# Optimization experiments

Hardware: AMD Instinct MI355X
Metric: run time of the kernel (lower is better)

The kernel has to match this reference:

```python
import jax, jax.numpy as jnp
import numpy as np

ATTEN_SIZE = 5  # half-window; module-global atten_size in source (0 there is non-functional)
B, S, D_IN, HID, OUT = 8, 2048, 512, 512, 2


def _xavier(key, shape):
    fan_in, fan_out = shape
    std = (2.0 / (fan_in + fan_out)) ** 0.5
    return jax.random.normal(key, shape, dtype=jnp.float32) * std


def setup_inputs() -> dict:
    key = jax.random.key(0)
    ks = jax.random.split(key, 8)
    return {
        "x": jax.random.normal(ks[0], (B, S, D_IN), dtype=jnp.float32),
        "W1": _xavier(ks[1], (D_IN, HID)),
        "b1": jnp.zeros((1, 1, HID), dtype=jnp.float32),
        "Wq": _xavier(ks[2], (HID, HID)),
        "Wk": _xavier(ks[3], (HID, HID)),
        "Wv": _xavier(ks[4], (HID, HID)),
        "W2": _xavier(ks[5], (HID, HID)),
        "b2": jnp.zeros((1, 1, HID), dtype=jnp.float32),
        "Wfc": _xavier(ks[6], (HID, OUT)),
        "bfc": jnp.zeros((OUT,), dtype=jnp.float32),
    }


def reference(x, W1, b1, Wq, Wk, Wv, W2, b2, Wfc, bfc):
    A = ATTEN_SIZE
    Wn = 2 * A + 1
    h = jax.nn.relu(x @ W1 + b1)                      # [B,S,H]
    b, s, hd = h.shape
    padded = jnp.pad(h, ((0, 0), (A, A), (0, 0)))     # [B,S+2A,H]
    # torch pad+roll(k)+stack+slice equals reversed window: x_nei[p, j] = padded[p + 2A - j]
    idx = jnp.arange(s)[:, None] + (2 * A - jnp.arange(Wn))[None, :]  # [S,Wn]
    x_nei = padded[:, idx, :]                         # [B,S,Wn,H]
    q = h @ Wq                                        # [B,S,H]
    k = x_nei @ Wk                                    # [B,S,Wn,H]
    v = x_nei @ Wv                                    # [B,S,Wn,H]
    scale = jnp.asarray(np.sqrt(float(hd)), dtype=h.dtype)
    scores = jnp.einsum('bsh,bswh->bsw', q, k)[:, :, None, :] / scale  # [B,S,1,Wn]
    # Faithful to torch.nn.Softmax(dim=2) on a singleton dim -> all ones
    w = jax.nn.softmax(scores, axis=2)                # [B,S,1,Wn]
    aw = jnp.einsum('bsjw,bswh->bsjh', w, v).reshape(b, s, hd)  # [B,S,H]
    out = jax.nn.relu(aw @ W2 + b2) @ Wfc + bfc       # [B,S,OUT]
    return out, aw
```

## Files before the change

kernel.cpp:

```cpp
#include <hip/hip_runtime.h>
#include <stdint.h>

#define B_   8
#define S_   2048
#define HID_ 512
#define M_   (B_ * S_)
#define AW_  5

typedef __attribute__((ext_vector_type(8))) short bf16x8;
typedef __attribute__((ext_vector_type(4))) float f32x4;
typedef unsigned short u16;

__device__ __forceinline__ u16 f2bf(float f) {
    uint32_t u = __builtin_bit_cast(uint32_t, f);
    u += 0x7FFFu + ((u >> 16) & 1u);
    return (u16)(u >> 16);
}
__device__ __forceinline__ float bf2f(u16 h) {
    uint32_t u = ((uint32_t)h) << 16;
    return __builtin_bit_cast(float, u);
}

__device__ __forceinline__ void gload16(const void* g, void* l) {
    __builtin_amdgcn_global_load_lds(
        (const __attribute__((address_space(1))) void*)(uintptr_t)g,
        (__attribute__((address_space(3))) void*)(uint32_t)(uintptr_t)l,
        16, 0, 0);
}

__global__ __launch_bounds__(256) void trans2w(const float* __restrict__ S0,
                                               const float* __restrict__ S1,
                                               u16* __restrict__ D0,
                                               u16* __restrict__ D1) {
    const float* src = blockIdx.z ? S1 : S0;
    u16* dst = blockIdx.z ? D1 : D0;
    __shared__ float tile[32][33];
    const int k0 = blockIdx.y * 32, n0 = blockIdx.x * 32;
    const int tr = threadIdx.x >> 5, tc = threadIdx.x & 31;
#pragma unroll
    for (int p = 0; p < 4; ++p)
        tile[tr + p * 8][tc] = src[(long)(k0 + tr + p * 8) * HID_ + n0 + tc];
    __syncthreads();
#pragma unroll
    for (int p = 0; p < 4; ++p)
        dst[(long)(n0 + tr + p * 8) * HID_ + k0 + tc] = f2bf(tile[tc][tr + p * 8]);
}

__global__ __launch_bounds__(256, 2) void gemm1_f32a(const float* __restrict__ A,
                                                     const u16* __restrict__ Bt,
                                                     const float* __restrict__ bias,
                                                     u16* __restrict__ C) {
    __shared__ __attribute__((aligned(16))) u16 As[2][128 * 64];
    __shared__ __attribute__((aligned(16))) u16 Bs[2][128 * 64];

    const int tid = threadIdx.x;
    const int bid = blockIdx.x;
    const int swz = (bid & 7) * 64 + (bid >> 3);
    const int  bn   = (swz & 3) * 128;
    const long brow = (long)(swz >> 2) * 128;

    const int w  = tid >> 6;
    const int l  = tid & 63;
    const int wm = (w >> 1) * 64;
    const int wn = (w & 1) * 64;
    const int lr  = l & 15;
    const int lkb = (l >> 4) * 16;
    const int sw  = (lr & 7) << 4;

    const int r0 = tid >> 2;
    const int c0 = (tid & 3) * 16;
    const int r1 = 64 + r0;
    const float* ga0 = A + (brow + r0) * 512 + c0;
    const float* ga1 = A + (brow + r1) * 512 + c0;
    char* lw = (char*)&As[0][0];
    const int wb00 = r0 * 128 + ((c0 * 2 +  0) ^ ((r0 & 7) << 4));
    const int wb01 = r0 * 128 + ((c0 * 2 + 16) ^ ((r0 & 7) << 4));
    const int wb10 = r1 * 128 + ((c0 * 2 +  0) ^ ((r1 & 7) << 4));
    const int wb11 = r1 * 128 + ((c0 * 2 + 16) ^ ((r1 & 7) << 4));

    int pq[4];
    const u16* srcB[4];
#pragma unroll
    for (int q = 0; q < 4; ++q) {
        const int p   = tid * 16 + q * 4096;
        const int row = p >> 7;
        const int cb  = (p & 127) ^ ((row & 7) << 4);
        pq[q]   = p;
        srcB[q] = Bt + (long)(bn + row) * 512 + (cb >> 1);
    }

    f32x4 acc[4][4];
#pragma unroll
    for (int i = 0; i < 4; ++i)
#pragma unroll
        for (int j = 0; j < 4; ++j) {
            f32x4 z = {0.f, 0.f, 0.f, 0.f};
            acc[i][j] = z;
        }

    float4 ra[4], rb[4];

#define LOADA(k0)                                                        \
    {                                                                    \
        _Pragma("unroll") for (int u = 0; u < 4; ++u) {                  \
            ra[u] = *(const float4*)(ga0 + (k0) + u * 4);                \
            rb[u] = *(const float4*)(ga1 + (k0) + u * 4);                \
        }                                                                \
    }
#define CVTWRITE(buf)                                                    \
    {                                                                    \
        union { u16 u[8]; int4 v; } q0, q1, q2, q3;                      \
        q0.u[0]=f2bf(ra[0].x); q0.u[1]=f2bf(ra[0].y); q0.u[2]=f2bf(ra[0].z); q0.u[3]=f2bf(ra[0].w); \
        q0.u[4]=f2bf(ra[1].x); q0.u[5]=f2bf(ra[1].y); q0.u[6]=f2bf(ra[1].z); q0.u[7]=f2bf(ra[1].w); \
        q1.u[0]=f2bf(ra[2].x); q1.u[1]=f2bf(ra[2].y); q1.u[2]=f2bf(ra[2].z); q1.u[3]=f2bf(ra[2].w); \
        q1.u[4]=f2bf(ra[3].x); q1.u[5]=f2bf(ra[3].y); q1.u[6]=f2bf(ra[3].z); q1.u[7]=f2bf(ra[3].w); \
        q2.u[0]=f2bf(rb[0].x); q2.u[1]=f2bf(rb[0].y); q2.u[2]=f2bf(rb[0].z); q2.u[3]=f2bf(rb[0].w); \
        q2.u[4]=f2bf(rb[1].x); q2.u[5]=f2bf(rb[1].y); q2.u[6]=f2bf(rb[1].z); q2.u[7]=f2bf(rb[1].w); \
        q3.u[0]=f2bf(rb[2].x); q3.u[1]=f2bf(rb[2].y); q3.u[2]=f2bf(rb[2].z); q3.u[3]=f2bf(rb[2].w); \
        q3.u[4]=f2bf(rb[3].x); q3.u[5]=f2bf(rb[3].y); q3.u[6]=f2bf(rb[3].z); q3.u[7]=f2bf(rb[3].w); \
        *(int4*)(lw + (buf) * 16384 + wb00) = q0.v;                      \
        *(int4*)(lw + (buf) * 16384 + wb01) = q1.v;                      \
        *(int4*)(lw + (buf) * 16384 + wb10) = q2.v;                      \
        *(int4*)(lw + (buf) * 16384 + wb11) = q3.v;                      \
    }
#define STAGEB(buf, k0)                                                  \
    {                                                                    \
        _Pragma("unroll") for (int q = 0; q < 4; ++q)                    \
            gload16(srcB[q] + (k0), (char*)&Bs[buf][0] + pq[q]);         \
    }

    LOADA(0);
    STAGEB(0, 0);
    CVTWRITE(0);
    __syncthreads();

    int cur = 0;
    for (int t = 0; t < 8; ++t) {
        if (t < 7) {
            LOADA((t + 1) * 64);
            STAGEB(cur ^ 1, (t + 1) * 64);
        }
#pragma unroll
        for (int kk = 0; kk < 2; ++kk) {
            bf16x8 af[4], bfr[4];
#pragma unroll
            for (int i = 0; i < 4; ++i) {
                const int off = (wm + i * 16 + lr) * 128 + ((kk * 64 + lkb) ^ sw);
                af[i] = *(const bf16x8*)((const char*)&As[cur][0] + off);
            }
#pragma unroll
            for (int j = 0; j < 4; ++j) {
                const int off = (wn + j * 16 + lr) * 128 + ((kk * 64 + lkb) ^ sw);
                bfr[j] = *(const bf16x8*)((const char*)&Bs[cur][0] + off);
            }
#pragma unroll
            for (int i = 0; i < 4; ++i)
#pragma unroll
                for (int j = 0; j < 4; ++j)
                    acc[i][j] = __builtin_amdgcn_mfma_f32_16x16x32_bf16(
                        af[i], bfr[j], acc[i][j], 0, 0, 0);
        }
        if (t < 7) CVTWRITE(cur ^ 1);
        __syncthreads();
        cur ^= 1;
    }
#undef LOADA
#undef CVTWRITE
#undef STAGEB

    float bv[4];
#pragma unroll
    for (int j = 0; j < 4; ++j) bv[j] = bias[bn + wn + j * 16 + lr];
    const int rq = (l >> 4) * 4;
#pragma unroll
    for (int i = 0; i < 4; ++i)
#pragma unroll
        for (int q = 0; q < 4; ++q) {
            const long row = brow + wm + i * 16 + rq + q;
            u16* crow = C + row * 512 + bn + wn + lr;
#pragma unroll
            for (int j = 0; j < 4; ++j)
                crow[j * 16] = f2bf(fmaxf(acc[i][j][q] + bv[j], 0.f));
        }
}

__global__ __launch_bounds__(256, 2) void gemm_bf16(const u16* __restrict__ A,
                                                    const u16* __restrict__ Bt,
                                                    u16* __restrict__ C) {
    __shared__ __attribute__((aligned(16))) u16 As[2][128 * 64];
    __shared__ __attribute__((aligned(16))) u16 Bs[2][128 * 64];

    const int tid = threadIdx.x;
    const int bid = blockIdx.x;
    const int swz = (bid & 7) * 64 + (bid >> 3);
    const int  bn   = (swz & 3) * 128;
    const long brow = (long)(swz >> 2) * 128;

    const int w  = tid >> 6;
    const int l  = tid & 63;
    const int wm = (w >> 1) * 64;
    const int wn = (w & 1) * 64;
    const int lr  = l & 15;
    const int lkb = (l >> 4) * 16;
    const int sw  = (lr & 7) << 4;

    int pq[4];
    const u16* srcA[4];
    const u16* srcB[4];
#pragma unroll
    for (int q = 0; q < 4; ++q) {
        const int p   = tid * 16 + q * 4096;
        const int row = p >> 7;
        const int cb  = (p & 127) ^ ((row & 7) << 4);
        pq[q]   = p;
        srcA[q] = A  + (brow + row) * 512 + (cb >> 1);
        srcB[q] = Bt + (long)(bn + row) * 512 + (cb >> 1);
    }

    f32x4 acc[4][4];
#pragma unroll
    for (int i = 0; i < 4; ++i)
#pragma unroll
        for (int j = 0; j < 4; ++j) {
            f32x4 z = {0.f, 0.f, 0.f, 0.f};
            acc[i][j] = z;
        }

#define STAGE(buf, k0)                                                   \
    {                                                                    \
        _Pragma("unroll") for (int q = 0; q < 4; ++q) {                  \
            gload16(srcA[q] + (k0), (char*)&As[buf][0] + pq[q]);         \
            gload16(srcB[q] + (k0), (char*)&Bs[buf][0] + pq[q]);         \
        }                                                                \
    }

    int cur = 0;
    STAGE(0, 0);
    __syncthreads();

    for (int t = 0; t < 8; ++t) {
        if (t < 7) STAGE(cur ^ 1, (t + 1) * 64);
#pragma unroll
        for (int kk = 0; kk < 2; ++kk) {
            bf16x8 af[4], bfr[4];
#pragma unroll
            for (int i = 0; i < 4; ++i) {
                const int off = (wm + i * 16 + lr) * 128 + ((kk * 64 + lkb) ^ sw);
                af[i] = *(const bf16x8*)((const char*)&As[cur][0] + off);
            }
#pragma unroll
            for (int j = 0; j < 4; ++j) {
                const int off = (wn + j * 16 + lr) * 128 + ((kk * 64 + lkb) ^ sw);
                bfr[j] = *(const bf16x8*)((const char*)&Bs[cur][0] + off);
            }
#pragma unroll
            for (int i = 0; i < 4; ++i)
#pragma unroll
                for (int j = 0; j < 4; ++j)
                    acc[i][j] = __builtin_amdgcn_mfma_f32_16x16x32_bf16(
                        af[i], bfr[j], acc[i][j], 0, 0, 0);
        }
        __syncthreads();
        cur ^= 1;
    }
#undef STAGE

    const int rq = (l >> 4) * 4;
#pragma unroll
    for (int i = 0; i < 4; ++i)
#pragma unroll
        for (int q = 0; q < 4; ++q) {
            const long row = brow + wm + i * 16 + rq + q;
            u16* crow = C + row * 512 + bn + wn + lr;
#pragma unroll
            for (int j = 0; j < 4; ++j)
                crow[j * 16] = f2bf(acc[i][j][q]);
        }
}

__global__ __launch_bounds__(256, 2) void gemm4_fc(const u16* __restrict__ A,
                                                   const u16* __restrict__ Bt,
                                                   const float* __restrict__ b2,
                                                   const float* __restrict__ Wfc,
                                                   float* __restrict__ partials) {
    __shared__ __attribute__((aligned(16))) u16 As[2][128 * 64];
    __shared__ __attribute__((aligned(16))) u16 Bs[2][128 * 64];

    const int tid = threadIdx.x;
    const int bid = blockIdx.x;
    const int swz = (bid & 7) * 64 + (bid >> 3);
    const int  bn   = (swz & 3) * 128;
    const long brow = (long)(swz >> 2) * 128;

    const int w  = tid >> 6;
    const int l  = tid & 63;
    const int wm = (w >> 1) * 64;
    const int wn = (w & 1) * 64;
    const int lr  = l & 15;
    const int lkb = (l >> 4) * 16;
    const int sw  = (lr & 7) << 4;

    int pq[4];
    const u16* srcA[4];
    const u16* srcB[4];
#pragma unroll
    for (int q = 0; q < 4; ++q) {
        const int p   = tid * 16 + q * 4096;
        const int row = p >> 7;
        const int cb  = (p & 127) ^ ((row & 7) << 4);
        pq[q]   = p;
        srcA[q] = A  + (brow + row) * 512 + (cb >> 1);
        srcB[q] = Bt + (long)(bn + row) * 512 + (cb >> 1);
    }

    f32x4 acc[4][4];
#pragma unroll
    for (int i = 0; i < 4; ++i)
#pragma unroll
        for (int j = 0; j < 4; ++j) {
            f32x4 z = {0.f, 0.f, 0.f, 0.f};
            acc[i][j] = z;
        }

#define STAGE(buf, k0)                                                   \
    {                                                                    \
        _Pragma("unroll") for (int q = 0; q < 4; ++q) {                  \
            gload16(srcA[q] + (k0), (char*)&As[buf][0] + pq[q]);         \
            gload16(srcB[q] + (k0), (char*)&Bs[buf][0] + pq[q]);         \
        }                                                                \
    }

    int cur = 0;
    STAGE(0, 0);
    __syncthreads();

    for (int t = 0; t < 8; ++t) {
        if (t < 7) STAGE(cur ^ 1, (t + 1) * 64);
#pragma unroll
        for (int kk = 0; kk < 2; ++kk) {
            bf16x8 af[4], bfr[4];
#pragma unroll
            for (int i = 0; i < 4; ++i) {
                const int off = (wm + i * 16 + lr) * 128 + ((kk * 64 + lkb) ^ sw);
                af[i] = *(const bf16x8*)((const char*)&As[cur][0] + off);
            }
#pragma unroll
            for (int j = 0; j < 4; ++j) {
                const int off = (wn + j * 16 + lr) * 128 + ((kk * 64 + lkb) ^ sw);
                bfr[j] = *(const bf16x8*)((const char*)&Bs[cur][0] + off);
            }
#pragma unroll
            for (int i = 0; i < 4; ++i)
#pragma unroll
                for (int j = 0; j < 4; ++j)
                    acc[i][j] = __builtin_amdgcn_mfma_f32_16x16x32_bf16(
                        af[i], bfr[j], acc[i][j], 0, 0, 0);
        }
        __syncthreads();
        cur ^= 1;
    }
#undef STAGE

    float bv[4], w0[4], w1[4];
#pragma unroll
    for (int j = 0; j < 4; ++j) {
        const int col = bn + wn + j * 16 + lr;
        bv[j] = b2[col];
        w0[j] = Wfc[2 * col];
        w1[j] = Wfc[2 * col + 1];
    }
    const int rq = (l >> 4) * 4;
    const int slot = (bn >> 7) * 2 + (wn >> 6);
#pragma unroll
    for (int i = 0; i < 4; ++i)
#pragma unroll
        for (int q = 0; q < 4; ++q) {
            float s0 = 0.f, s1 = 0.f;
#pragma unroll
            for (int j = 0; j < 4; ++j) {
                const float v = fmaxf(acc[i][j][q] + bv[j], 0.f);
                s0 += v * w0[j];
                s1 += v * w1[j];
            }
#pragma unroll
            for (int m = 1; m < 16; m <<= 1) {
                s0 += __shfl_xor(s0, m);
                s1 += __shfl_xor(s1, m);
            }
            if (lr == 0) {
                const long row = brow + wm + i * 16 + rq + q;
                float* pp = partials + ((long)slot * M_ + row) * 2;
                pp[0] = s0;
                pp[1] = s1;
            }
        }
}

__global__ __launch_bounds__(256) void winsum_f(const u16* __restrict__ g,
                                                u16* __restrict__ awb,
                                                float* __restrict__ awf) {
    const long idx = (long)blockIdx.x * 256 + threadIdx.x;
    const int  c8  = (int)(idx & 63);
    const long bs  = idx >> 6;
    const int  s   = (int)(bs & (S_ - 1));

    float acc[8] = {};
#pragma unroll
    for (int d = -AW_; d <= AW_; ++d) {
        const int ss = s + d;
        if (0 <= ss && ss < S_) {
            const int4 v = *(const int4*)&g[(bs + d) * HID_ + c8 * 8];
            const u16* u = (const u16*)&v;
#pragma unroll
            for (int e = 0; e < 8; ++e) acc[e] += bf2f(u[e]);
        }
    }
    union { u16 u[8]; int4 v; } r;
#pragma unroll
    for (int e = 0; e < 8; ++e) r.u[e] = f2bf(acc[e]);
    *(int4*)&awb[bs * HID_ + c8 * 8] = r.v;
    float4 o0 = {acc[0], acc[1], acc[2], acc[3]};
    float4 o1 = {acc[4], acc[5], acc[6], acc[7]};
    *(float4*)&awf[bs * HID_ + c8 * 8]     = o0;
    *(float4*)&awf[bs * HID_ + c8 * 8 + 4] = o1;
}

__global__ __launch_bounds__(256) void fc_reduce(const float* __restrict__ partials,
                                                 const float* __restrict__ bfc,
                                                 float* __restrict__ out) {
    const int row = blockIdx.x * 256 + threadIdx.x;
    float s0 = bfc[0], s1 = bfc[1];
#pragma unroll
    for (int p = 0; p < 8; ++p) {
        s0 += partials[((long)p * M_ + row) * 2 + 0];
        s1 += partials[((long)p * M_ + row) * 2 + 1];
    }
    out[row * 2 + 0] = s0;
    out[row * 2 + 1] = s1;
}

extern "C" void kernel_launch(void* const* d_in, const int* in_sizes, int n_in,
                              void* d_out, int out_size, void* d_ws, size_t ws_size,
                              hipStream_t stream) {
    const float* x   = (const float*)d_in[0];
    const float* W1  = (const float*)d_in[1];
    const float* b1  = (const float*)d_in[2];
    const float* Wv  = (const float*)d_in[5];
    const float* W2  = (const float*)d_in[6];
    const float* b2  = (const float*)d_in[7];
    const float* Wfc = (const float*)d_in[8];
    const float* bfc = (const float*)d_in[9];

    float* out_part = (float*)d_out;
    float* aw_f32   = (float*)d_out + (long)M_ * 2;

    u16* W1t = (u16*)aw_f32;
    u16* Wvt = W1t + 262144;

    u16* h   = (u16*)d_ws;
    u16* g   = (u16*)d_ws + 8388608;
    u16* awb = h;
    u16* W2t = g;
    float* partials = (float*)((char*)d_ws + 16 * 1024 * 1024 + 512 * 1024);

    trans2w<<<dim3(16, 16, 2), 256, 0, stream>>>(W1, Wv, W1t, Wvt);
    gemm1_f32a<<<512, 256, 0, stream>>>(x, W1t, b1, h);
    gemm_bf16<<<512, 256, 0, stream>>>(h, Wvt, g);
    winsum_f<<<4096, 256, 0, stream>>>(g, awb, aw_f32);
    trans2w<<<dim3(16, 16, 1), 256, 0, stream>>>(W2, W2, W2t, W2t);
    gemm4_fc<<<512, 256, 0, stream>>>(awb, W2t, b2, Wfc, partials);
    fc_reduce<<<64, 256, 0, stream>>>(partials, bfc, out_part);
}
```

Before: 78.79 us.

## Triple-buffer bf16 GEMMs with 64x128 tiles and fuse weight prep

The two bf16 GEMMs (the h·Wv projection and the W2+FC epilogue) are merged into one templated kernel. It uses 64x128 block tiles, 1024 blocks, and a three-stage LDS pipeline synchronised with explicit vmcnt/lgkmcnt waits and raw barriers instead of __syncthreads. All three weight transposes are folded into a single prep kernel when the workspace is large enough, which removes a launch mid-pipeline. Partials grow to 16 slots because each wave now owns 32 columns, so fc_reduce sums more terms. The smaller tiles raise occupancy and overlap but lower the MFMA-to-load ratio.

```diff
diff --git a/kernel.cpp b/kernel.cpp
--- a/kernel.cpp
+++ b/kernel.cpp
@@ -28,22 +28,45 @@
         16, 0, 0);
 }
 
-__global__ __launch_bounds__(256) void trans2w(const float* __restrict__ S0,
-                                               const float* __restrict__ S1,
-                                               u16* __restrict__ D0,
-                                               u16* __restrict__ D1) {
-    const float* src = blockIdx.z ? S1 : S0;
-    u16* dst = blockIdx.z ? D1 : D0;
+#define WAITV(n)  asm volatile("s_waitcnt vmcnt(" #n ")" ::: "memory")
+#define WAITLG0() asm volatile("s_waitcnt lgkmcnt(0)" ::: "memory")
+
+__global__ __launch_bounds__(256) void prep_w(const float* __restrict__ W1,
+                                              const float* __restrict__ Wv,
+                                              const float* __restrict__ W2,
+                                              u16* __restrict__ W1t,
+                                              u16* __restrict__ Wvt,
+                                              u16* __restrict__ W2t,
+                                              int do_w2) {
+    const int wsel = blockIdx.x >> 8;
+    if (wsel == 2 && !do_w2) return;
+    const float* src = wsel == 0 ? W1 : (wsel == 1 ? Wv : W2);
+    u16* dst = wsel == 0 ? W1t : (wsel == 1 ? Wvt : W2t);
+    const int t  = blockIdx.x & 255;
+    const int n0 = (t & 15) * 32, k0 = (t >> 4) * 32;
+    __shared__ float tile[32][33];
+    const int tr = threadIdx.x >> 5, tc = threadIdx.x & 31;
+#pragma unroll
+    for (int p = 0; p < 4; ++p)
+        tile[tr + p * 8][tc] = src[(long)(k0 + tr + p * 8) * HID_ + n0 + tc];
+    __syncthreads();
+#pragma unroll
+    for (int p = 0; p < 4; ++p)
+        dst[(long)(n0 + tr + p * 8) * HID_ + k0 + tc] = f2bf(tile[tc][tr + p * 8]);
+}
+
+__global__ __launch_bounds__(256) void trans_w2(const float* __restrict__ W2,
+                                                u16* __restrict__ W2t) {
     __shared__ float tile[32][33];
     const int k0 = blockIdx.y * 32, n0 = blockIdx.x * 32;
     const int tr = threadIdx.x >> 5, tc = threadIdx.x & 31;
 #pragma unroll
     for (int p = 0; p < 4; ++p)
-        tile[tr + p * 8][tc] = src[(long)(k0 + tr + p * 8) * HID_ + n0 + tc];
+        tile[tr + p * 8][tc] = W2[(long)(k0 + tr + p * 8) * HID_ + n0 + tc];
     __syncthreads();
 #pragma unroll
     for (int p = 0; p < 4; ++p)
-        dst[(long)(n0 + tr + p * 8) * HID_ + k0 + tc] = f2bf(tile[tc][tr + p * 8]);
+        W2t[(long)(n0 + tr + p * 8) * HID_ + k0 + tc] = f2bf(tile[tc][tr + p * 8]);
 }
 
 __global__ __launch_bounds__(256, 2) void gemm1_f32a(const float* __restrict__ A,
@@ -184,216 +207,164 @@
         }
 }
 
-__global__ __launch_bounds__(256, 2) void gemm_bf16(const u16* __restrict__ A,
+template <int EPI>
+__global__ __launch_bounds__(256, 2) void gemm_pipe(const u16* __restrict__ A,
                                                     const u16* __restrict__ Bt,
-                                                    u16* __restrict__ C) {
-    __shared__ __attribute__((aligned(16))) u16 As[2][128 * 64];
-    __shared__ __attribute__((aligned(16))) u16 Bs[2][128 * 64];
+                                                    const float* __restrict__ b2,
+                                                    const float* __restrict__ Wfc,
+                                                    u16* __restrict__ C,
+                                                    float* __restrict__ partials) {
+    __shared__ __attribute__((aligned(16))) u16 As[3][64 * 64];
+    __shared__ __attribute__((aligned(16))) u16 Bs[3][128 * 64];
 
     const int tid = threadIdx.x;
     const int bid = blockIdx.x;
-    const int swz = (bid & 7) * 64 + (bid >> 3);
+    const int swz = (bid & 7) * 128 + (bid >> 3);
     const int  bn   = (swz & 3) * 128;
-    const long brow = (long)(swz >> 2) * 128;
+    const long brow = (long)(swz >> 2) * 64;
 
     const int w  = tid >> 6;
     const int l  = tid & 63;
-    const int wm = (w >> 1) * 64;
-    const int wn = (w & 1) * 64;
+    const int wn = w * 32;
     const int lr  = l & 15;
     const int lkb = (l >> 4) * 16;
     const int sw  = (lr & 7) << 4;
 
-    int pq[4];
-    const u16* srcA[4];
+    int pa[2], pb[4];
+    const u16* srcA[2];
     const u16* srcB[4];
+#pragma unroll
+    for (int q = 0; q < 2; ++q) {
+        const int p   = tid * 16 + q * 4096;
+        const int row = p >> 7;
+        const int cb  = (p & 127) ^ ((row & 7) << 4);
+        pa[q]   = p;
+        srcA[q] = A + (brow + row) * 512 + (cb >> 1);
+    }
 #pragma unroll
     for (int q = 0; q < 4; ++q) {
         const int p   = tid * 16 + q * 4096;
         const int row = p >> 7;
         const int cb  = (p & 127) ^ ((row & 7) << 4);
-        pq[q]   = p;
-        srcA[q] = A  + (brow + row) * 512 + (cb >> 1);
+        pb[q]   = p;
         srcB[q] = Bt + (long)(bn + row) * 512 + (cb >> 1);
     }
 
-    f32x4 acc[4][4];
+    f32x4 acc[4][2];
 #pragma unroll
     for (int i = 0; i < 4; ++i)
 #pragma unroll
-        for (int j = 0; j < 4; ++j) {
+        for (int j = 0; j < 2; ++j) {
             f32x4 z = {0.f, 0.f, 0.f, 0.f};
             acc[i][j] = z;
         }
 
-#define STAGE(buf, k0)                                                   \
+#define STAGEP(buf, k0)                                                  \
     {                                                                    \
-        _Pragma("unroll") for (int q = 0; q < 4; ++q) {                  \
-            gload16(srcA[q] + (k0), (char*)&As[buf][0] + pq[q]);         \
-            gload16(srcB[q] + (k0), (char*)&Bs[buf][0] + pq[q]);         \
-        }                                                                \
-    }
-
-    int cur = 0;
-    STAGE(0, 0);
-    __syncthreads();
-
+        gload16(srcA[0] + (k0), (char*)&As[buf][0] + pa[0]);             \
+        gload16(srcA[1] + (k0), (char*)&As[buf][0] + pa[1]);             \
+        gload16(srcB[0] + (k0), (char*)&Bs[buf][0] + pb[0]);             \
+        gload16(srcB[1] + (k0), (char*)&Bs[buf][0] + pb[1]);             \
+        gload16(srcB[2] + (k0), (char*)&Bs[buf][0] + pb[2]);             \
+        gload16(srcB[3] + (k0), (char*)&Bs[buf][0] + pb[3]);             \
+    }
+
+    STAGEP(0, 0);
+    STAGEP(1, 64);
+    WAITV(6);
+    __builtin_amdgcn_s_barrier();
+
+#pragma unroll
     for (int t = 0; t < 8; ++t) {
-        if (t < 7) STAGE(cur ^ 1, (t + 1) * 64);
+        if (t < 6) {
+            const int nb = (t + 2) % 3;
+            if (nb == 0)      STAGEP(0, (t + 2) * 64)
+            else if (nb == 1) STAGEP(1, (t + 2) * 64)
+            else              STAGEP(2, (t + 2) * 64)
+        }
+
+        const int cb = t % 3;
+        const char* ab = cb == 0 ? (const char*)&As[0][0]
+                       : cb == 1 ? (const char*)&As[1][0] : (const char*)&As[2][0];
+        const char* bb = cb == 0 ? (const char*)&Bs[0][0]
+                       : cb == 1 ? (const char*)&Bs[1][0] : (const char*)&Bs[2][0];
 #pragma unroll
         for (int kk = 0; kk < 2; ++kk) {
-            bf16x8 af[4], bfr[4];
+            bf16x8 af[4], bfr[2];
 #pragma unroll
             for (int i = 0; i < 4; ++i) {
-                const int off = (wm + i * 16 + lr) * 128 + ((kk * 64 + lkb) ^ sw);
-                af[i] = *(const bf16x8*)((const char*)&As[cur][0] + off);
-            }
-#pragma unroll
-            for (int j = 0; j < 4; ++j) {
+                const int off = (i * 16 + lr) * 128 + ((kk * 64 + lkb) ^ sw);
+                af[i] = *(const bf16x8*)(ab + off);
+            }
+#pragma unroll
+            for (int j = 0; j < 2; ++j) {
                 const int off = (wn + j * 16 + lr) * 128 + ((kk * 64 + lkb) ^ sw);
-                bfr[j] = *(const bf16x8*)((const char*)&Bs[cur][0] + off);
+                bfr[j] = *(const bf16x8*)(bb + off);
             }
 #pragma unroll
             for (int i = 0; i < 4; ++i)
 #pragma unroll
-                for (int j = 0; j < 4; ++j)
+                for (int j = 0; j < 2; ++j)
                     acc[i][j] = __builtin_amdgcn_mfma_f32_16x16x32_bf16(
                         af[i], bfr[j], acc[i][j], 0, 0, 0);
         }
-        __syncthreads();
-        cur ^= 1;
-    }
-#undef STAGE
+
+        if (t < 7) {
+            WAITLG0();
+            __builtin_amdgcn_sched_barrier(0);
+            if (t < 6) WAITV(6);
+            else       WAITV(0);
+            __builtin_amdgcn_s_barrier();
+        }
+    }
+#undef STAGEP
 
     const int rq = (l >> 4) * 4;
-#pragma unroll
-    for (int i = 0; i < 4; ++i)
-#pragma unroll
-        for (int q = 0; q < 4; ++q) {
-            const long row = brow + wm + i * 16 + rq + q;
-            u16* crow = C + row * 512 + bn + wn + lr;
-#pragma unroll
-            for (int j = 0; j < 4; ++j)
-                crow[j * 16] = f2bf(acc[i][j][q]);
-        }
-}
-
-__global__ __launch_bounds__(256, 2) void gemm4_fc(const u16* __restrict__ A,
-                                                   const u16* __restrict__ Bt,
-                                                   const float* __restrict__ b2,
-                                                   const float* __restrict__ Wfc,
-                                                   float* __restrict__ partials) {
-    __shared__ __attribute__((aligned(16))) u16 As[2][128 * 64];
-    __shared__ __attribute__((aligned(16))) u16 Bs[2][128 * 64];
-
-    const int tid = threadIdx.x;
-    const int bid = blockIdx.x;
-    const int swz = (bid & 7) * 64 + (bid >> 3);
-    const int  bn   = (swz & 3) * 128;
-    const long brow = (long)(swz >> 2) * 128;
-
-    const int w  = tid >> 6;
-    const int l  = tid & 63;
-    const int wm = (w >> 1) * 64;
-    const int wn = (w & 1) * 64;
-    const int lr  = l & 15;
-    const int lkb = (l >> 4) * 16;
-    const int sw  = (lr & 7) << 4;
-
-    int pq[4];
-    const u16* srcA[4];
-    const u16* srcB[4];
-#pragma unroll
-    for (int q = 0; q < 4; ++q) {
-        const int p   = tid * 16 + q * 4096;
-        const int row = p >> 7;
-        const int cb  = (p & 127) ^ ((row & 7) << 4);
-        pq[q]   = p;
-        srcA[q] = A  + (brow + row) * 512 + (cb >> 1);
-        srcB[q] = Bt + (long)(bn + row) * 512 + (cb >> 1);
-    }
-
-    f32x4 acc[4][4];
-#pragma unroll
-    for (int i = 0; i < 4; ++i)
-#pragma unroll
-        for (int j = 0; j < 4; ++j) {
-            f32x4 z = {0.f, 0.f, 0.f, 0.f};
-            acc[i][j] = z;
-        }
-
-#define STAGE(buf, k0)                                                   \
-    {                                                                    \
-        _Pragma("unroll") for (int q = 0; q < 4; ++q) {                  \
-            gload16(srcA[q] + (k0), (char*)&As[buf][0] + pq[q]);         \
-            gload16(srcB[q] + (k0), (char*)&Bs[buf][0] + pq[q]);         \
-        }                                                                \
-    }
-
-    int cur = 0;
-    STAGE(0, 0);
-    __syncthreads();
-
-    for (int t = 0; t < 8; ++t) {
-        if (t < 7) STAGE(cur ^ 1, (t + 1) * 64);
-#pragma unroll
-        for (int kk = 0; kk < 2; ++kk) {
-            bf16x8 af[4], bfr[4];
-#pragma unroll
-            for (int i = 0; i < 4; ++i) {
-                const int off = (wm + i * 16 + lr) * 128 + ((kk * 64 + lkb) ^ sw);
-                af[i] = *(const bf16x8*)((const char*)&As[cur][0] + off);
-            }
-#pragma unroll
-            for (int j = 0; j < 4; ++j) {
-                const int off = (wn + j * 16 + lr) * 128 + ((kk * 64 + lkb) ^ sw);
-                bfr[j] = *(const bf16x8*)((const char*)&Bs[cur][0] + off);
-            }
-#pragma unroll
-            for (int i = 0; i < 4; ++i)
-#pragma unroll
-                for (int j = 0; j < 4; ++j)
-                    acc[i][j] = __builtin_amdgcn_mfma_f32_16x16x32_bf16(
-                        af[i], bfr[j], acc[i][j], 0, 0, 0);
-        }
-        __syncthreads();
-        cur ^= 1;
-    }
-#undef STAGE
-
-    float bv[4], w0[4], w1[4];
-#pragma unroll
-    for (int j = 0; j < 4; ++j) {
-        const int col = bn + wn + j * 16 + lr;
-        bv[j] = b2[col];
-        w0[j] = Wfc[2 * col];
-        w1[j] = Wfc[2 * col + 1];
-    }
-    const int rq = (l >> 4) * 4;
-    const int slot = (bn >> 7) * 2 + (wn >> 6);
-#pragma unroll
-    for (int i = 0; i < 4; ++i)
-#pragma unroll
-        for (int q = 0; q < 4; ++q) {
-            float s0 = 0.f, s1 = 0.f;
-#pragma unroll
-            for (int j = 0; j < 4; ++j) {
-                const float v = fmaxf(acc[i][j][q] + bv[j], 0.f);
-                s0 += v * w0[j];
-                s1 += v * w1[j];
-            }
-#pragma unroll
-            for (int m = 1; m < 16; m <<= 1) {
-                s0 += __shfl_xor(s0, m);
-                s1 += __shfl_xor(s1, m);
-            }
-            if (lr == 0) {
-                const long row = brow + wm + i * 16 + rq + q;
-                float* pp = partials + ((long)slot * M_ + row) * 2;
-                pp[0] = s0;
-                pp[1] = s1;
-            }
-        }
+    if (EPI == 0) {
+#pragma unroll
+        for (int i = 0; i < 4; ++i)
+#pragma unroll
+            for (int q = 0; q < 4; ++q) {
+                const long row = brow + i * 16 + rq + q;
+                u16* crow = C + row * 512 + bn + wn + lr;
+#pragma unroll
+                for (int j = 0; j < 2; ++j)
+                    crow[j * 16] = f2bf(acc[i][j][q]);
+            }
+    } else {
+        float bvv[2], w0v[2], w1v[2];
+#pragma unroll
+        for (int j = 0; j < 2; ++j) {
+            const int col = bn + wn + j * 16 + lr;
+            bvv[j] = b2[col];
+            w0v[j] = Wfc[2 * col];
+            w1v[j] = Wfc[2 * col + 1];
+        }
+        const int slot = (bn >> 7) * 4 + w;
+#pragma unroll
+        for (int i = 0; i < 4; ++i)
+#pragma unroll
+            for (int q = 0; q < 4; ++q) {
+                float s0 = 0.f, s1 = 0.f;
+#pragma unroll
+                for (int j = 0; j < 2; ++j) {
+                    const float v = fmaxf(acc[i][j][q] + bvv[j], 0.f);
+                    s0 += v * w0v[j];
+                    s1 += v * w1v[j];
+                }
+#pragma unroll
+                for (int m = 1; m < 16; m <<= 1) {
+                    s0 += __shfl_xor(s0, m);
+                    s1 += __shfl_xor(s1, m);
+                }
+                if (lr == 0) {
+                    const long row = brow + i * 16 + rq + q;
+                    float* pp = partials + ((long)slot * M_ + row) * 2;
+                    pp[0] = s0;
+                    pp[1] = s1;
+                }
+            }
+    }
 }
 
 __global__ __launch_bounds__(256) void winsum_f(const u16* __restrict__ g,
@@ -431,7 +402,7 @@
     const int row = blockIdx.x * 256 + threadIdx.x;
     float s0 = bfc[0], s1 = bfc[1];
 #pragma unroll
-    for (int p = 0; p < 8; ++p) {
+    for (int p = 0; p < 16; ++p) {
         s0 += partials[((long)p * M_ + row) * 2 + 0];
         s1 += partials[((long)p * M_ + row) * 2 + 1];
     }
@@ -454,20 +425,25 @@
     float* out_part = (float*)d_out;
     float* aw_f32   = (float*)d_out + (long)M_ * 2;
 
+    unsigned char* ws = (unsigned char*)d_ws;
+
     u16* W1t = (u16*)aw_f32;
     u16* Wvt = W1t + 262144;
 
-    u16* h   = (u16*)d_ws;
-    u16* g   = (u16*)d_ws + 8388608;
+    u16* h   = (u16*)ws;
+    u16* g   = (u16*)ws + 8388608;
     u16* awb = h;
-    u16* W2t = g;
-    float* partials = (float*)((char*)d_ws + 16 * 1024 * 1024 + 512 * 1024);
-
-    trans2w<<<dim3(16, 16, 2), 256, 0, stream>>>(W1, Wv, W1t, Wvt);
+    float* partials = (float*)(ws + (17l << 20));
+
+    const bool big = ws_size >= ((size_t)34 << 20);
+    u16* W2t = big ? (u16*)(ws + (33l << 20)) : g;
+
+    prep_w<<<768, 256, 0, stream>>>(W1, Wv, W2, W1t, Wvt, W2t, big ? 1 : 0);
     gemm1_f32a<<<512, 256, 0, stream>>>(x, W1t, b1, h);
-    gemm_bf16<<<512, 256, 0, stream>>>(h, Wvt, g);
+    gemm_pipe<0><<<1024, 256, 0, stream>>>(h, Wvt, nullptr, nullptr, g, nullptr);
     winsum_f<<<4096, 256, 0, stream>>>(g, awb, aw_f32);
-    trans2w<<<dim3(16, 16, 1), 256, 0, stream>>>(W2, W2, W2t, W2t);
-    gemm4_fc<<<512, 256, 0, stream>>>(awb, W2t, b2, Wfc, partials);
+    if (!big)
+        trans_w2<<<dim3(16, 16), 256, 0, stream>>>(W2, W2t);
+    gemm_pipe<1><<<1024, 256, 0, stream>>>(awb, W2t, b2, Wfc, nullptr, partials);
     fc_reduce<<<64, 256, 0, stream>>>(partials, bfc, out_part);
 }
```

Result: slower. 83.97 us (+6.6%).
